# Kernel tuning notes

Measured on AMD Instinct MI355X. Metric: run time of the kernel, lower is better.

The kernel has to match this reference:

```python
import jax, jax.numpy as jnp
import numpy as np

N_NODES = 100000


def gcn_conv(x, edge_index, edge_weight, W, b, num_nodes):
    """PyG-style GCNConv: add self-loops, symmetric normalization, aggregate, linear."""
    src, dst = edge_index[0], edge_index[1]
    loop = jnp.arange(num_nodes, dtype=src.dtype)
    src_f = jnp.concatenate([src, loop])
    dst_f = jnp.concatenate([dst, loop])
    w_f = jnp.concatenate([edge_weight, jnp.ones((num_nodes,), dtype=edge_weight.dtype)])

    # symmetric normalization D^-1/2 A_hat D^-1/2
    deg = jax.ops.segment_sum(w_f, dst_f, num_segments=num_nodes)
    dinv = jnp.where(deg > 0, jax.lax.rsqrt(deg), 0.0)
    norm = dinv[src_f] * w_f * dinv[dst_f]  # [E + N]

    h = x @ W  # transform first (small out dim) -> cheaper gather/scatter
    msg = h[src_f] * norm[:, None]  # [E + N, out]
    out = jax.ops.segment_sum(msg, dst_f, num_segments=num_nodes)
    return out + b


def setup_inputs() -> dict:
    key = jax.random.key(0)
    k = jax.random.split(key, 7)
    N, E, F, H, C = N_NODES, 3200000, 64, 32, 5
    x = jax.random.normal(k[0], (N, F), dtype=jnp.float32)
    edge_index = jax.random.randint(k[1], (2, E), 0, N, dtype=jnp.int64)
    edge_attr = jax.random.uniform(k[2], (E,), dtype=jnp.float32)
    # Glorot-style init for GCNConv weights, zero bias (PyG default)
    W1 = jax.random.normal(k[3], (F, H), dtype=jnp.float32) * (1.0 / np.sqrt(F))
    b1 = jnp.zeros((H,), dtype=jnp.float32)
    W2 = jax.random.normal(k[4], (H, C), dtype=jnp.float32) * (1.0 / np.sqrt(H))
    b2 = jnp.zeros((C,), dtype=jnp.float32)
    return {"x": x, "edge_index": edge_index, "edge_attr": edge_attr,
            "W1": W1, "b1": b1, "W2": W2, "b2": b2}


def reference(x, edge_index, edge_attr, W1, b1, W2, b2):
    # Dropout is identity in eval mode.
    x1 = gcn_conv(x, edge_index, edge_attr, W1, b1, N_NODES)
    x1 = jax.nn.relu(x1)
    x2 = gcn_conv(x1, edge_index, edge_attr, W2, b2, N_NODES)
    return (x2, x1)
```

## Files before the change

kernel.cpp:

```cpp
#include <hip/hip_runtime.h>

#define NN 100000
#define NE 3200000
#define FIN 64
#define FH 32
#define FO 5
#define NB 1000
#define NPB 100
#define NBIN (4*NPB)
#define QDIV 25000
#define GC 512
#define EPB (NE/GC)
#define KPT 25
#define CAP 3584
#define WQS 32767.f
#define WQI (1.0f/32767.f)

__device__ __forceinline__ int detect64(const int* __restrict__ ei, int* sflag, int tid) {
    if (tid < 64) {
        int v = ei[2 * tid + 1];
        unsigned long long m = __ballot(v == 0);
        if (tid == 0) *sflag = (m == ~0ULL) ? 1 : 0;
    }
    __syncthreads();
    return *sflag;
}

__device__ __forceinline__ unsigned bf16r(float f) {
    unsigned u = __float_as_uint(f);
    return (u + 0x7FFFu + ((u >> 16) & 1u)) >> 16;
}
__device__ __forceinline__ float blo(unsigned u) { return __uint_as_float(u << 16); }
__device__ __forceinline__ float bhi(unsigned u) { return __uint_as_float(u & 0xFFFF0000u); }

__global__ void k_fillC(const int* __restrict__ ei, const float* __restrict__ w,
                        int* __restrict__ cntRM, int* __restrict__ locRM,
                        int2* __restrict__ edata) {
    __shared__ unsigned stage_a[EPB];
    __shared__ unsigned stage_w[EPB];
    __shared__ int hist[NB];
    __shared__ int hoff[NB];
    __shared__ int sscan[256];
    __shared__ int sflag;
    int tid = threadIdx.x, g = blockIdx.x;
    for (int i = tid; i < NB; i += 256) hist[i] = 0;
    int is64 = detect64(ei, &sflag, tid);
    __syncthreads();
    int base = g * EPB;
    int myd[KPT];
#pragma unroll
    for (int k = 0; k < KPT; ++k) {
        int e = base + tid + k * 256;
        int dst = -1;
        if (e < base + EPB) {
            dst = is64 ? ei[2 * NE + 2 * e] : ei[NE + e];
            atomicAdd(&hist[dst / NPB], 1);
        }
        myd[k] = dst;
    }
    __syncthreads();
    for (int i = tid; i < NB; i += 256) cntRM[g * NB + i] = hist[i];
    int b0 = tid * 4;
    int c0 = (b0 + 0 < NB) ? hist[b0 + 0] : 0;
    int c1 = (b0 + 1 < NB) ? hist[b0 + 1] : 0;
    int c2 = (b0 + 2 < NB) ? hist[b0 + 2] : 0;
    int c3 = (b0 + 3 < NB) ? hist[b0 + 3] : 0;
    sscan[tid] = c0 + c1 + c2 + c3;
    __syncthreads();
    for (int off = 1; off < 256; off <<= 1) {
        int v = (tid >= off) ? sscan[tid - off] : 0;
        __syncthreads();
        sscan[tid] += v;
        __syncthreads();
    }
    int excl = sscan[tid] - (c0 + c1 + c2 + c3);
    if (b0 + 0 < NB) { hoff[b0 + 0] = excl;                locRM[g * NB + b0 + 0] = excl; }
    if (b0 + 1 < NB) { hoff[b0 + 1] = excl + c0;           locRM[g * NB + b0 + 1] = excl + c0; }
    if (b0 + 2 < NB) { hoff[b0 + 2] = excl + c0 + c1;      locRM[g * NB + b0 + 2] = excl + c0 + c1; }
    if (b0 + 3 < NB) { hoff[b0 + 3] = excl + c0 + c1 + c2; locRM[g * NB + b0 + 3] = excl + c0 + c1 + c2; }
    __syncthreads();
#pragma unroll
    for (int k = 0; k < KPT; ++k) {
        int e = base + tid + k * 256;
        if (e < base + EPB) {
            int src = is64 ? ei[2 * e] : ei[e];
            int dst = myd[k];
            int b = dst / NPB;
            int dloc = dst - b * NPB;
            int pos = atomicAdd(&hoff[b], 1);
            stage_a[pos] = (unsigned)(src | (dloc << 20));
            stage_w[pos] = __float_as_uint(w[e]);
        }
    }
    __syncthreads();
    int4* go = (int4*)(edata + (size_t)g * EPB);
    for (int i = tid; i < EPB / 2; i += 256) {
        int4 v;
        v.x = (int)stage_a[2 * i];     v.y = (int)stage_w[2 * i];
        v.z = (int)stage_a[2 * i + 1]; v.w = (int)stage_w[2 * i + 1];
        go[i] = v;
    }
}

__global__ __launch_bounds__(512) void k_nodecsr(
        const int* __restrict__ cntRM, const int* __restrict__ locRM,
        const int2* __restrict__ edata, unsigned* __restrict__ edata2,
        int* __restrict__ rowS, int* __restrict__ rowE, float* __restrict__ dinv) {
    __shared__ unsigned s1a[CAP];
    __shared__ unsigned char s1d[CAP];
    __shared__ unsigned s2a[CAP];
    __shared__ int cnt[NBIN];
    __shared__ int loc[NBIN];
    __shared__ int cur[NBIN];
    __shared__ int sc[512];
    __shared__ int sBlen;
    int b = blockIdx.x, tid = threadIdx.x;
    int base = b * CAP;
    int g = tid;
    int len  = cntRM[g * NB + b];
    int gsrc = g * EPB + locRM[g * NB + b];
    for (int i = tid; i < NBIN; i += 512) cnt[i] = 0;
    sc[tid] = len;
    __syncthreads();
    for (int off = 1; off < 512; off <<= 1) {
        int x = (tid >= off) ? sc[tid - off] : 0;
        __syncthreads();
        sc[tid] += x;
        __syncthreads();
    }
    int sdst = sc[tid] - len;
    if (tid == 511) sBlen = sc[511];
    __syncthreads();
    int blen = sBlen;
    if (blen <= CAP) {
        for (int k = 0; k < len; ++k) {
            int2 e = edata[gsrc + k];
            unsigned a = (unsigned)e.x;
            int dloc = a >> 20, src = (int)(a & 0xFFFFF);
            unsigned wq = (unsigned)(__int_as_float(e.y) * WQS + 0.5f);
            atomicAdd(&cnt[(dloc << 2) | (src / QDIV)], 1);
            s1a[sdst + k] = (unsigned)src | (wq << 17);
            s1d[sdst + k] = (unsigned char)dloc;
        }
        __syncthreads();
        int v = (tid < NBIN) ? cnt[tid] : 0;
        sc[tid] = v;
        __syncthreads();
        for (int off = 1; off < 512; off <<= 1) {
            int x = (tid >= off) ? sc[tid - off] : 0;
            __syncthreads();
            sc[tid] += x;
            __syncthreads();
        }
        if (tid < NBIN) { loc[tid] = sc[tid] - v; cur[tid] = sc[tid] - v; }
        __syncthreads();
        if (tid < NPB) {
            rowS[b * NPB + tid] = base + loc[4 * tid];
            rowE[b * NPB + tid] = base + ((tid == NPB - 1) ? blen : loc[4 * tid + 4]);
        }
        for (int j = tid; j < blen; j += 512) {
            unsigned a = s1a[j];
            int dloc = s1d[j];
            int src = (int)(a & 0x1FFFF);
            int pos = atomicAdd(&cur[(dloc << 2) | (src / QDIV)], 1);
            s2a[pos] = a;
        }
        __syncthreads();
        if (tid < NPB) {
            int e0 = loc[4 * tid];
            int e1 = (tid == NPB - 1) ? blen : loc[4 * tid + 4];
            int isum = 0;
            for (int j = e0; j < e1; ++j) isum += (int)(s2a[j] >> 17);
            dinv[b * NPB + tid] = rsqrtf(1.0f + (float)isum * WQI);
        }
        for (int j = tid; j < blen; j += 512) edata2[base + j] = s2a[j];
    } else {
        float* degL = (float*)s1a;
        if (tid < NPB) degL[tid] = 0.f;
        __syncthreads();
        for (int k = 0; k < len; ++k) {
            int2 e = edata[gsrc + k];
            unsigned a = (unsigned)e.x;
            int dloc = a >> 20, src = (int)(a & 0xFFFFF);
            atomicAdd(&cnt[(dloc << 2) | (src / QDIV)], 1);
            atomicAdd(&degL[dloc], __int_as_float(e.y));
        }
        __syncthreads();
        int v = (tid < NBIN) ? cnt[tid] : 0;
        sc[tid] = v;
        __syncthreads();
        for (int off = 1; off < 512; off <<= 1) {
            int x = (tid >= off) ? sc[tid - off] : 0;
            __syncthreads();
            sc[tid] += x;
            __syncthreads();
        }
        if (tid < NBIN) { loc[tid] = sc[tid] - v; cur[tid] = base + sc[tid] - v; }
        __syncthreads();
        if (tid < NPB) {
            int e1 = (tid == NPB - 1) ? blen : loc[4 * tid + 4];
            if (e1 > CAP) e1 = CAP;
            int e0 = loc[4 * tid]; if (e0 > CAP) e0 = CAP;
            rowS[b * NPB + tid] = base + e0;
            rowE[b * NPB + tid] = base + e1;
            dinv[b * NPB + tid] = rsqrtf(1.0f + degL[tid]);
        }
        __syncthreads();
        for (int k = 0; k < len; ++k) {
            int2 e = edata[gsrc + k];
            unsigned a = (unsigned)e.x;
            int dloc = a >> 20, src = (int)(a & 0xFFFFF);
            unsigned wq = (unsigned)(__int_as_float(e.y) * WQS + 0.5f);
            int pos = atomicAdd(&cur[(dloc << 2) | (src / QDIV)], 1);
            if (pos < base + CAP) edata2[pos] = (unsigned)src | (wq << 17);
        }
    }
}

__global__ void k_gemm1(const float* __restrict__ x, const float* __restrict__ W1,
                        const float* __restrict__ dinv, unsigned* __restrict__ hs1b) {
    __shared__ float Ws[FIN * FH];
    __shared__ float Xs[16 * FIN];
    int tid = threadIdx.x;
    for (int i = tid; i < FIN * FH; i += 256) Ws[i] = W1[i];
    int row0 = blockIdx.x * 16;
    for (int i = tid; i < 16 * FIN; i += 256) Xs[i] = x[row0 * FIN + i];
    __syncthreads();
    int l = tid & 15, r = tid >> 4;
    int n = row0 + r;
    float a0 = 0.f, a1 = 0.f;
    const float* xr = &Xs[r * FIN];
#pragma unroll
    for (int f = 0; f < FIN; ++f) {
        float xv = xr[f];
        a0 += xv * Ws[f * FH + 2 * l];
        a1 += xv * Ws[f * FH + 2 * l + 1];
    }
    float di = dinv[n];
    hs1b[n * 16 + l] = bf16r(di * a0) | (bf16r(di * a1) << 16);
}

__global__ void k_pull1(const int* __restrict__ rowS, const int* __restrict__ rowE,
                        const unsigned* __restrict__ ed,
                        const unsigned* __restrict__ hs1b, const float* __restrict__ dinv,
                        const float* __restrict__ b1, const float* __restrict__ W2,
                        float* __restrict__ x1out, unsigned* __restrict__ hs2b) {
    __shared__ float Ws2[FH * FO];
    int tid = threadIdx.x;
    if (tid < FH * FO) Ws2[tid] = W2[tid];
    __syncthreads();
    int l = tid & 15;
    int n = blockIdx.x * 16 + (tid >> 4);
    int s = rowS[n], t = rowE[n];
    unsigned su = hs1b[n * 16 + l];
    float a0 = blo(su), a1 = bhi(su);
    int i = s;
    for (; i + 8 <= t; i += 8) {
        unsigned c0 = ed[i],     c1 = ed[i + 1], c2 = ed[i + 2], c3 = ed[i + 3];
        unsigned c4 = ed[i + 4], c5 = ed[i + 5], c6 = ed[i + 6], c7 = ed[i + 7];
        unsigned u0 = hs1b[(c0 & 0x1FFFF) * 16 + l];
        unsigned u1 = hs1b[(c1 & 0x1FFFF) * 16 + l];
        unsigned u2 = hs1b[(c2 & 0x1FFFF) * 16 + l];
        unsigned u3 = hs1b[(c3 & 0x1FFFF) * 16 + l];
        unsigned u4 = hs1b[(c4 & 0x1FFFF) * 16 + l];
        unsigned u5 = hs1b[(c5 & 0x1FFFF) * 16 + l];
        unsigned u6 = hs1b[(c6 & 0x1FFFF) * 16 + l];
        unsigned u7 = hs1b[(c7 & 0x1FFFF) * 16 + l];
        float w0 = (float)(c0 >> 17) * WQI, w1 = (float)(c1 >> 17) * WQI;
        float w2 = (float)(c2 >> 17) * WQI, w3 = (float)(c3 >> 17) * WQI;
        float w4 = (float)(c4 >> 17) * WQI, w5 = (float)(c5 >> 17) * WQI;
        float w6 = (float)(c6 >> 17) * WQI, w7 = (float)(c7 >> 17) * WQI;
        a0 += w0 * blo(u0); a1 += w0 * bhi(u0);
        a0 += w1 * blo(u1); a1 += w1 * bhi(u1);
        a0 += w2 * blo(u2); a1 += w2 * bhi(u2);
        a0 += w3 * blo(u3); a1 += w3 * bhi(u3);
        a0 += w4 * blo(u4); a1 += w4 * bhi(u4);
        a0 += w5 * blo(u5); a1 += w5 * bhi(u5);
        a0 += w6 * blo(u6); a1 += w6 * bhi(u6);
        a0 += w7 * blo(u7); a1 += w7 * bhi(u7);
    }
    for (; i < t; ++i) {
        unsigned c = ed[i];
        unsigned u = hs1b[(c & 0x1FFFF) * 16 + l];
        float we = (float)(c >> 17) * WQI;
        a0 += we * blo(u); a1 += we * bhi(u);
    }
    float di = dinv[n];
    float v0 = di * a0 + b1[2 * l];
    float v1 = di * a1 + b1[2 * l + 1];
    v0 = (v0 > 0.f) ? v0 : 0.f;
    v1 = (v1 > 0.f) ? v1 : 0.f;
    float2 st; st.x = v0; st.y = v1;
    *(float2*)&x1out[n * FH + 2 * l] = st;
    float hv[6];
    hv[5] = 0.f;
#pragma unroll
    for (int c = 0; c < FO; ++c) {
        float pr = v0 * Ws2[(2 * l) * FO + c] + v1 * Ws2[(2 * l + 1) * FO + c];
        pr += __shfl_xor(pr, 1, 16);
        pr += __shfl_xor(pr, 2, 16);
        pr += __shfl_xor(pr, 4, 16);
        pr += __shfl_xor(pr, 8, 16);
        hv[c] = di * pr;
    }
    if (l < 3) hs2b[n * 4 + l] = bf16r(hv[2 * l]) | (bf16r(hv[2 * l + 1]) << 16);
}

__global__ void k_pull2(const int* __restrict__ rowS, const int* __restrict__ rowE,
                        const unsigned* __restrict__ ed,
                        const unsigned* __restrict__ hs2b, const float* __restrict__ dinv,
                        const float* __restrict__ b2, float* __restrict__ out) {
    int tid = threadIdx.x;
    int c = tid & 7;
    int cm = (c < FO) ? c : 0;
    int wj = cm >> 1, hh = cm & 1;
    int n = blockIdx.x * 32 + (tid >> 3);
    int s = rowS[n], t = rowE[n];
    unsigned us = hs2b[n * 4 + wj];
    float acc = hh ? bhi(us) : blo(us);
    int i = s;
    for (; i + 4 <= t; i += 4) {
        unsigned c0 = ed[i], c1 = ed[i + 1], c2 = ed[i + 2], c3 = ed[i + 3];
        unsigned u0 = hs2b[(c0 & 0x1FFFF) * 4 + wj];
        unsigned u1 = hs2b[(c1 & 0x1FFFF) * 4 + wj];
        unsigned u2 = hs2b[(c2 & 0x1FFFF) * 4 + wj];
        unsigned u3 = hs2b[(c3 & 0x1FFFF) * 4 + wj];
        float v0 = hh ? bhi(u0) : blo(u0);
        float v1 = hh ? bhi(u1) : blo(u1);
        float v2 = hh ? bhi(u2) : blo(u2);
        float v3 = hh ? bhi(u3) : blo(u3);
        acc += (float)(c0 >> 17) * WQI * v0;
        acc += (float)(c1 >> 17) * WQI * v1;
        acc += (float)(c2 >> 17) * WQI * v2;
        acc += (float)(c3 >> 17) * WQI * v3;
    }
    for (; i < t; ++i) {
        unsigned cc = ed[i];
        unsigned u = hs2b[(cc & 0x1FFFF) * 4 + wj];
        acc += (float)(cc >> 17) * WQI * (hh ? bhi(u) : blo(u));
    }
    if (c < FO) out[n * FO + c] = dinv[n] * acc + b2[c];
}

extern "C" void kernel_launch(void* const* d_in, const int* in_sizes, int n_in,
                              void* d_out, int out_size, void* d_ws, size_t ws_size,
                              hipStream_t stream) {
    const float* x  = (const float*)d_in[0];
    const int*   ei = (const int*)d_in[1];
    const float* w  = (const float*)d_in[2];
    const float* W1 = (const float*)d_in[3];
    const float* b1 = (const float*)d_in[4];
    const float* W2 = (const float*)d_in[5];
    const float* b2 = (const float*)d_in[6];
    float* out = (float*)d_out;
    float* ws  = (float*)d_ws;

    int2*     edata  = (int2*)ws;
    unsigned* edata2 = (unsigned*)(ws + 6400000);
    float*    dinv   = ws + 10000000;
    int*      rowS   = (int*)(ws + 10100000);
    int*      rowE   = (int*)(ws + 10200000);
    int*      cntRM  = (int*)(ws + 12800000);
    int*      locRM  = (int*)(ws + 13312000);
    unsigned* hs1b   = (unsigned*)ws;
    unsigned* hs2b   = (unsigned*)(ws + 1600000);

    float* x1 = out + NN * FO;

    k_fillC<<<GC, 256, 0, stream>>>(ei, w, cntRM, locRM, edata);
    k_nodecsr<<<NB, 512, 0, stream>>>(cntRM, locRM, edata, edata2, rowS, rowE, dinv);
    k_gemm1<<<NN / 16, 256, 0, stream>>>(x, W1, dinv, hs1b);
    k_pull1<<<NN / 16, 256, 0, stream>>>(rowS, rowE, edata2, hs1b, dinv, b1, W2, x1, hs2b);
    k_pull2<<<NN / 32, 256, 0, stream>>>(rowS, rowE, edata2, hs2b, dinv, b2, out);
}
```

Before: 247.5 us.

## Pack quantized edge data into 4+1 byte streams and swizzle CSR block order

The first binning pass now quantizes edge weights and packs src plus weight into one 32-bit word, with the local destination kept in a separate byte array. This replaces the 8-byte int2 intermediate, cutting the write and read traffic between the two CSR-building kernels. The node-CSR kernel also remaps block indices in an interleaved pattern, and the second pull loop is unrolled to 8 gathers for more memory-level parallelism. The overflow path now accumulates degree from quantized integer weights instead of float weights, which slightly changes precision.

```diff
diff --git a/kernel.cpp b/kernel.cpp
--- a/kernel.cpp
+++ b/kernel.cpp
@@ -12,6 +12,8 @@
 #define GC 512
 #define EPB (NE/GC)
 #define KPT 25
+#define APAD 6252
+#define DPAD 6272
 #define CAP 3584
 #define WQS 32767.f
 #define WQI (1.0f/32767.f)
@@ -35,9 +37,9 @@
 
 __global__ void k_fillC(const int* __restrict__ ei, const float* __restrict__ w,
                         int* __restrict__ cntRM, int* __restrict__ locRM,
-                        int2* __restrict__ edata) {
+                        unsigned* __restrict__ edata_a, unsigned char* __restrict__ edata_d) {
     __shared__ unsigned stage_a[EPB];
-    __shared__ unsigned stage_w[EPB];
+    __shared__ unsigned char stage_d[EPB];
     __shared__ int hist[NB];
     __shared__ int hoff[NB];
     __shared__ int sscan[256];
@@ -87,24 +89,38 @@
             int dst = myd[k];
             int b = dst / NPB;
             int dloc = dst - b * NPB;
+            unsigned wq = (unsigned)(w[e] * WQS + 0.5f);
             int pos = atomicAdd(&hoff[b], 1);
-            stage_a[pos] = (unsigned)(src | (dloc << 20));
-            stage_w[pos] = __float_as_uint(w[e]);
-        }
-    }
-    __syncthreads();
-    int4* go = (int4*)(edata + (size_t)g * EPB);
-    for (int i = tid; i < EPB / 2; i += 256) {
+            stage_a[pos] = (unsigned)src | (wq << 17);
+            stage_d[pos] = (unsigned char)dloc;
+        }
+    }
+    __syncthreads();
+    unsigned* ga = edata_a + (size_t)g * APAD;
+    int4* ga4 = (int4*)ga;
+    const int NI4 = EPB / 4;
+    for (int i = tid; i < NI4; i += 256) {
         int4 v;
-        v.x = (int)stage_a[2 * i];     v.y = (int)stage_w[2 * i];
-        v.z = (int)stage_a[2 * i + 1]; v.w = (int)stage_w[2 * i + 1];
-        go[i] = v;
+        v.x = (int)stage_a[4 * i];     v.y = (int)stage_a[4 * i + 1];
+        v.z = (int)stage_a[4 * i + 2]; v.w = (int)stage_a[4 * i + 3];
+        ga4[i] = v;
+    }
+    if (tid < EPB - NI4 * 4) ga[NI4 * 4 + tid] = stage_a[NI4 * 4 + tid];
+    unsigned* gd = (unsigned*)(edata_d + (size_t)g * DPAD);
+    const int ND = (EPB + 3) / 4;
+    for (int i = tid; i < ND; i += 256) {
+        unsigned b0v = stage_d[4 * i];
+        unsigned b1v = (4 * i + 1 < EPB) ? stage_d[4 * i + 1] : 0;
+        unsigned b2v = (4 * i + 2 < EPB) ? stage_d[4 * i + 2] : 0;
+        unsigned b3v = (4 * i + 3 < EPB) ? stage_d[4 * i + 3] : 0;
+        gd[i] = b0v | (b1v << 8) | (b2v << 16) | (b3v << 24);
     }
 }
 
 __global__ __launch_bounds__(512) void k_nodecsr(
         const int* __restrict__ cntRM, const int* __restrict__ locRM,
-        const int2* __restrict__ edata, unsigned* __restrict__ edata2,
+        const unsigned* __restrict__ edata_a, const unsigned char* __restrict__ edata_d,
+        unsigned* __restrict__ edata2,
         int* __restrict__ rowS, int* __restrict__ rowE, float* __restrict__ dinv) {
     __shared__ unsigned s1a[CAP];
     __shared__ unsigned char s1d[CAP];
@@ -114,11 +130,14 @@
     __shared__ int cur[NBIN];
     __shared__ int sc[512];
     __shared__ int sBlen;
-    int b = blockIdx.x, tid = threadIdx.x;
+    int bi = blockIdx.x, tid = threadIdx.x;
+    int b = (bi & 7) * (NB / 8) + (bi >> 3);
     int base = b * CAP;
     int g = tid;
     int len  = cntRM[g * NB + b];
-    int gsrc = g * EPB + locRM[g * NB + b];
+    int lloc = locRM[g * NB + b];
+    const unsigned* A = edata_a + (size_t)g * APAD + lloc;
+    const unsigned char* D = edata_d + (size_t)g * DPAD + lloc;
     for (int i = tid; i < NBIN; i += 512) cnt[i] = 0;
     sc[tid] = len;
     __syncthreads();
@@ -134,12 +153,11 @@
     int blen = sBlen;
     if (blen <= CAP) {
         for (int k = 0; k < len; ++k) {
-            int2 e = edata[gsrc + k];
-            unsigned a = (unsigned)e.x;
-            int dloc = a >> 20, src = (int)(a & 0xFFFFF);
-            unsigned wq = (unsigned)(__int_as_float(e.y) * WQS + 0.5f);
+            unsigned a = A[k];
+            int dloc = D[k];
+            int src = (int)(a & 0x1FFFF);
             atomicAdd(&cnt[(dloc << 2) | (src / QDIV)], 1);
-            s1a[sdst + k] = (unsigned)src | (wq << 17);
+            s1a[sdst + k] = a;
             s1d[sdst + k] = (unsigned char)dloc;
         }
         __syncthreads();
@@ -175,15 +193,15 @@
         }
         for (int j = tid; j < blen; j += 512) edata2[base + j] = s2a[j];
     } else {
-        float* degL = (float*)s1a;
-        if (tid < NPB) degL[tid] = 0.f;
+        int* degI = (int*)s1a;
+        if (tid < NPB) degI[tid] = 0;
         __syncthreads();
         for (int k = 0; k < len; ++k) {
-            int2 e = edata[gsrc + k];
-            unsigned a = (unsigned)e.x;
-            int dloc = a >> 20, src = (int)(a & 0xFFFFF);
+            unsigned a = A[k];
+            int dloc = D[k];
+            int src = (int)(a & 0x1FFFF);
             atomicAdd(&cnt[(dloc << 2) | (src / QDIV)], 1);
-            atomicAdd(&degL[dloc], __int_as_float(e.y));
+            atomicAdd(&degI[dloc], (int)(a >> 17));
         }
         __syncthreads();
         int v = (tid < NBIN) ? cnt[tid] : 0;
@@ -203,16 +221,15 @@
             int e0 = loc[4 * tid]; if (e0 > CAP) e0 = CAP;
             rowS[b * NPB + tid] = base + e0;
             rowE[b * NPB + tid] = base + e1;
-            dinv[b * NPB + tid] = rsqrtf(1.0f + degL[tid]);
+            dinv[b * NPB + tid] = rsqrtf(1.0f + (float)degI[tid] * WQI);
         }
         __syncthreads();
         for (int k = 0; k < len; ++k) {
-            int2 e = edata[gsrc + k];
-            unsigned a = (unsigned)e.x;
-            int dloc = a >> 20, src = (int)(a & 0xFFFFF);
-            unsigned wq = (unsigned)(__int_as_float(e.y) * WQS + 0.5f);
+            unsigned a = A[k];
+            int dloc = D[k];
+            int src = (int)(a & 0x1FFFF);
             int pos = atomicAdd(&cur[(dloc << 2) | (src / QDIV)], 1);
-            if (pos < base + CAP) edata2[pos] = (unsigned)src | (wq << 17);
+            if (pos < base + CAP) edata2[pos] = a;
         }
     }
 }
@@ -319,20 +336,25 @@
     unsigned us = hs2b[n * 4 + wj];
     float acc = hh ? bhi(us) : blo(us);
     int i = s;
-    for (; i + 4 <= t; i += 4) {
-        unsigned c0 = ed[i], c1 = ed[i + 1], c2 = ed[i + 2], c3 = ed[i + 3];
+    for (; i + 8 <= t; i += 8) {
+        unsigned c0 = ed[i],     c1 = ed[i + 1], c2 = ed[i + 2], c3 = ed[i + 3];
+        unsigned c4 = ed[i + 4], c5 = ed[i + 5], c6 = ed[i + 6], c7 = ed[i + 7];
         unsigned u0 = hs2b[(c0 & 0x1FFFF) * 4 + wj];
         unsigned u1 = hs2b[(c1 & 0x1FFFF) * 4 + wj];
         unsigned u2 = hs2b[(c2 & 0x1FFFF) * 4 + wj];
         unsigned u3 = hs2b[(c3 & 0x1FFFF) * 4 + wj];
-        float v0 = hh ? bhi(u0) : blo(u0);
-        float v1 = hh ? bhi(u1) : blo(u1);
-        float v2 = hh ? bhi(u2) : blo(u2);
-        float v3 = hh ? bhi(u3) : blo(u3);
-        acc += (float)(c0 >> 17) * WQI * v0;
-        acc += (float)(c1 >> 17) * WQI * v1;
-        acc += (float)(c2 >> 17) * WQI * v2;
-        acc += (float)(c3 >> 17) * WQI * v3;
+        unsigned u4 = hs2b[(c4 & 0x1FFFF) * 4 + wj];
+        unsigned u5 = hs2b[(c5 & 0x1FFFF) * 4 + wj];
+        unsigned u6 = hs2b[(c6 & 0x1FFFF) * 4 + wj];
+        unsigned u7 = hs2b[(c7 & 0x1FFFF) * 4 + wj];
+        acc += (float)(c0 >> 17) * WQI * (hh ? bhi(u0) : blo(u0));
+        acc += (float)(c1 >> 17) * WQI * (hh ? bhi(u1) : blo(u1));
+        acc += (float)(c2 >> 17) * WQI * (hh ? bhi(u2) : blo(u2));
+        acc += (float)(c3 >> 17) * WQI * (hh ? bhi(u3) : blo(u3));
+        acc += (float)(c4 >> 17) * WQI * (hh ? bhi(u4) : blo(u4));
+        acc += (float)(c5 >> 17) * WQI * (hh ? bhi(u5) : blo(u5));
+        acc += (float)(c6 >> 17) * WQI * (hh ? bhi(u6) : blo(u6));
+        acc += (float)(c7 >> 17) * WQI * (hh ? bhi(u7) : blo(u7));
     }
     for (; i < t; ++i) {
         unsigned cc = ed[i];
@@ -355,20 +377,21 @@
     float* out = (float*)d_out;
     float* ws  = (float*)d_ws;
 
-    int2*     edata  = (int2*)ws;
-    unsigned* edata2 = (unsigned*)(ws + 6400000);
-    float*    dinv   = ws + 10000000;
-    int*      rowS   = (int*)(ws + 10100000);
-    int*      rowE   = (int*)(ws + 10200000);
-    int*      cntRM  = (int*)(ws + 12800000);
-    int*      locRM  = (int*)(ws + 13312000);
-    unsigned* hs1b   = (unsigned*)ws;
-    unsigned* hs2b   = (unsigned*)(ws + 1600000);
+    unsigned*      edata_a = (unsigned*)ws;
+    unsigned char* edata_d = (unsigned char*)(ws + 3300000);
+    unsigned*      edata2  = (unsigned*)(ws + 6400000);
+    float*         dinv    = ws + 10000000;
+    int*           rowS    = (int*)(ws + 10100000);
+    int*           rowE    = (int*)(ws + 10200000);
+    int*           cntRM   = (int*)(ws + 12800000);
+    int*           locRM   = (int*)(ws + 13312000);
+    unsigned*      hs1b    = (unsigned*)ws;
+    unsigned*      hs2b    = (unsigned*)(ws + 1600000);
 
     float* x1 = out + NN * FO;
 
-    k_fillC<<<GC, 256, 0, stream>>>(ei, w, cntRM, locRM, edata);
-    k_nodecsr<<<NB, 512, 0, stream>>>(cntRM, locRM, edata, edata2, rowS, rowE, dinv);
+    k_fillC<<<GC, 256, 0, stream>>>(ei, w, cntRM, locRM, edata_a, edata_d);
+    k_nodecsr<<<NB, 512, 0, stream>>>(cntRM, locRM, edata_a, edata_d, edata2, rowS, rowE, dinv);
     k_gemm1<<<NN / 16, 256, 0, stream>>>(x, W1, dinv, hs1b);
     k_pull1<<<NN / 16, 256, 0, stream>>>(rowS, rowE, edata2, hs1b, dinv, b1, W2, x1, hs2b);
     k_pull2<<<NN / 32, 256, 0, stream>>>(rowS, rowE, edata2, hs2b, dinv, b2, out);
```

Result: faster. 237.9 us (-3.9%).
